# Kernel optimization log

Measured on AMD Instinct MI355X. Metric: run time of the kernel, lower is better.

Reference implementation:

```python
import jax, jax.numpy as jnp
import numpy as np

B, N, D = 4, 8192, 1024
H, DK = 8, 128          # d_k = D // H
FF = 4096
EPS = 1e-5


def setup_inputs() -> dict:
    key = jax.random.key(0)
    ks = jax.random.split(key, 8)
    s = 0.02  # init scale for weights
    return {
        "x": jax.random.normal(ks[0], (B, N, D), jnp.float32),
        "delta_x": jax.random.uniform(ks[1], (N,), jnp.float32),
        # Linear weights stored [in, out] (math-equivalent to torch's x @ W.T)
        "Wq": jax.random.normal(ks[2], (D, D), jnp.float32) * s,
        "bq": jnp.zeros((D,), jnp.float32),
        "Wk": jax.random.normal(ks[3], (D, D), jnp.float32) * s,
        "bk": jnp.zeros((D,), jnp.float32),
        "Wv": jax.random.normal(ks[4], (D, D), jnp.float32) * s,
        "bv": jnp.zeros((D,), jnp.float32),
        # per-head LayerNorm params for K; NOTE: the original code (faithfully
        # reproduced) applies layernorms_K to BOTH key and value in Galerkin mode.
        "gamma_k": jnp.ones((H, DK), jnp.float32),
        "beta_k": jnp.zeros((H, DK), jnp.float32),
        "W1": jax.random.normal(ks[5], (D, FF), jnp.float32) * s,
        "b1": jnp.zeros((FF,), jnp.float32),
        "W2": jax.random.normal(ks[6], (FF, D), jnp.float32) * s,
        "b2": jnp.zeros((D,), jnp.float32),
    }


def _per_head_ln(t, gamma, beta):
    # t: [B, H, N, DK]; torch LayerNorm: biased variance over last dim
    mu = jnp.mean(t, axis=-1, keepdims=True)
    var = jnp.mean(jnp.square(t - mu), axis=-1, keepdims=True)
    t = (t - mu) * jax.lax.rsqrt(var + EPS)
    return t * gamma[None, :, None, :] + beta[None, :, None, :]


def reference(x, delta_x, Wq, bq, Wk, bk, Wv, bv, gamma_k, beta_k, W1, b1, W2, b2):
    b, n, d = x.shape

    def heads(y):  # [b, n, d] -> [b, H, n, DK]
        return y.reshape(b, n, H, DK).transpose(0, 2, 1, 3)

    q = heads(x @ Wq + bq)
    k = heads(x @ Wk + bk)
    v = heads(x @ Wv + bv)

    k = _per_head_ln(k, gamma_k, beta_k)
    v = _per_head_ln(v, gamma_k, beta_k)  # layernorms_K reused on value (as in source)
    k = k * delta_x[None, None, :, None]  # einsum('bhxd,x->bhxd')

    # Galerkin (softmax-free, linear) attention: (K^T V) / N then Q @ (.)
    scores = jnp.einsum("bhnd,bhne->bhde", k, v) / n  # [b,H,DK,DK]
    attn_out = jnp.einsum("bhnd,bhde->bhne", q, scores)  # [b,H,n,DK]
    # (F.dropout in the source treated as identity: inference/eval semantics)

    x = x + attn_out.transpose(0, 2, 1, 3).reshape(b, n, d)  # residual 1
    h = jax.nn.silu(x @ W1 + b1)
    return x + (h @ W2 + b2)  # residual 2
```

## Files before the change

### kernel.cpp

```cpp
#include <hip/hip_runtime.h>
#include <hip/hip_bf16.h>
#include <stdint.h>

#define DEV __device__ __forceinline__

typedef __attribute__((ext_vector_type(8))) short bf16x8;
typedef __attribute__((ext_vector_type(8))) unsigned short u16x8;
typedef __attribute__((ext_vector_type(4))) unsigned short u16x4;
typedef __attribute__((ext_vector_type(4))) float f32x4;

static constexpr int BB = 4, NN = 8192, DD = 1024, HH = 8, DKK = 128, FFF = 4096;
static constexpr int MM = BB * NN;

DEV float bfb2f(unsigned int s) { unsigned int x = s << 16; float f; __builtin_memcpy(&f, &x, 4); return f; }
DEV unsigned short f2bfb(float f) {
    unsigned int x; __builtin_memcpy(&x, &f, 4);
    x += 0x7fffu + ((x >> 16) & 1u);
    return (unsigned short)(x >> 16);
}

DEV void gload_lds16(const void* g, void* l) {
    auto gp = (const __attribute__((address_space(1))) void*)(uintptr_t)g;
    auto lp = (__attribute__((address_space(3))) void*)(unsigned int)(uintptr_t)l;
    __builtin_amdgcn_global_load_lds(gp, lp, 16, 0, 0);
}

__global__ void k_pack_bf16(const float* __restrict__ in, unsigned short* __restrict__ ob, long n) {
    long i = ((long)blockIdx.x * blockDim.x + threadIdx.x) * 8;
    if (i >= n) return;
    f32x4 a = *(const f32x4*)&in[i];
    f32x4 b = *(const f32x4*)&in[i + 4];
    u16x8 o;
    o[0]=f2bfb(a[0]); o[1]=f2bfb(a[1]); o[2]=f2bfb(a[2]); o[3]=f2bfb(a[3]);
    o[4]=f2bfb(b[0]); o[5]=f2bfb(b[1]); o[6]=f2bfb(b[2]); o[7]=f2bfb(b[3]);
    *(u16x8*)&ob[i] = o;
}

DEV void transpose_body(const float* __restrict__ W, unsigned short* __restrict__ WT, int R, int C,
                        int bx, int by, int tid) {
    __shared__ float t[32][33];
    const int r0 = by * 32, c0 = bx * 32;
    const int lr = tid >> 3, lc = (tid & 7) * 4;
    f32x4 v = *(const f32x4*)&W[(long)(r0 + lr) * C + c0 + lc];
    t[lr][lc + 0] = v[0]; t[lr][lc + 1] = v[1]; t[lr][lc + 2] = v[2]; t[lr][lc + 3] = v[3];
    __syncthreads();
    const int oc = tid >> 3, orr = (tid & 7) * 4;
    u16x4 o;
    o[0] = f2bfb(t[orr + 0][oc]); o[1] = f2bfb(t[orr + 1][oc]);
    o[2] = f2bfb(t[orr + 2][oc]); o[3] = f2bfb(t[orr + 3][oc]);
    *(u16x4*)&WT[(long)(c0 + oc) * R + r0 + orr] = o;
}
__global__ void k_transpose(const float* __restrict__ W, unsigned short* __restrict__ WT, int R, int C) {
    transpose_body(W, WT, R, C, blockIdx.x, blockIdx.y, threadIdx.x);
}
__global__ void k_transpose_qkv(const float* __restrict__ Wq, const float* __restrict__ Wk,
                                const float* __restrict__ Wv, unsigned short* __restrict__ WT) {
    const float* W = blockIdx.z == 0 ? Wq : (blockIdx.z == 1 ? Wk : Wv);
    transpose_body(W, WT + (size_t)blockIdx.z * DD * DD, DD, DD, blockIdx.x, blockIdx.y, threadIdx.x);
}

template <int EPI>
__global__ __launch_bounds__(512, 2)
void k_gemm256(const unsigned short* __restrict__ A, int lda,
               const unsigned short* __restrict__ BT, int ldbt,
               const float* __restrict__ bias0, const float* __restrict__ bias1,
               const float* __restrict__ bias2,
               const unsigned short* __restrict__ resb,
               unsigned short* __restrict__ outp0, unsigned short* __restrict__ outp1,
               unsigned short* __restrict__ outp2,
               float* __restrict__ outf,
               int K, int gridx, int npass)
{
    extern __shared__ __align__(128) unsigned short smem[];
    unsigned short* As = smem;
    unsigned short* Bs = smem + 4 * 8192;

    const int wg0 = (blockIdx.x & 7) * 32 + (blockIdx.x >> 3);

    const int tid = threadIdx.x;
    const int lane = tid & 63;
    const int w = tid >> 6;
    const int wm = w >> 2, wn = w & 3;
    const int fr = lane & 15;
    const int kg = lane >> 4;

    const int dl = tid * 16;
    const int soff = dl ^ (((dl >> 7) & 3) << 4);
    const int arow = soff >> 6;
    const int akel = (soff & 63) >> 1;

    int aoff[8], boff[4];
    #pragma unroll
    for (int m = 0; m < 8; ++m) { int o = (wm * 128 + m * 16 + fr) * 64 + kg * 16; aoff[m] = o ^ (((o >> 7) & 3) << 4); }
    #pragma unroll
    for (int n = 0; n < 4; ++n) { int o = (wn * 64 + n * 16 + fr) * 64 + kg * 16; boff[n] = o ^ (((o >> 7) & 3) << 4); }

#define STG_A(base, u, ks, slot) do { \
        const unsigned short* _g = (base) + (long)(u) * 64 + (ks) * 32; \
        gload_lds16(_g,              (slot) + tid * 8); \
        gload_lds16(_g + 128L * lda, (slot) + 4096 + tid * 8); } while (0)
#define STG_B(base, u, ks, slot) do { \
        const unsigned short* _g = (base) + (long)(u) * 64 + (ks) * 32; \
        gload_lds16(_g,               (slot) + tid * 8); \
        gload_lds16(_g + 128L * ldbt, (slot) + 4096 + tid * 8); } while (0)

#define BAR() __builtin_amdgcn_s_barrier()
#define VM8() asm volatile("s_waitcnt vmcnt(8)" ::: "memory")

#define MFMA16(AF, BF, R0) do { \
        __builtin_amdgcn_s_setprio(1); \
        _Pragma("unroll") \
        for (int m = 0; m < 4; ++m) { \
            _Pragma("unroll") \
            for (int n = 0; n < 4; ++n) \
                acc[(R0) + m][n] = __builtin_amdgcn_mfma_f32_16x16x32_bf16(AF[m], BF[n], acc[(R0) + m][n], 0, 0, 0); \
        } \
        __builtin_amdgcn_s_setprio(0); } while (0)

#define DO_TILE(sa0, sa1, sb0, sb1, STG0, STG1, STG2, STG3) do { \
        bf16x8 b0f[4], a0f[4], a1f[4], b1f[4], a2f[4], a3f[4]; \
        _Pragma("unroll") \
        for (int n = 0; n < 4; ++n) b0f[n] = *(const bf16x8*)((const char*)(sb0) + boff[n]); \
        _Pragma("unroll") \
        for (int m = 0; m < 4; ++m) a0f[m] = *(const bf16x8*)((const char*)(sa0) + aoff[m]); \
        _Pragma("unroll") \
        for (int m = 0; m < 4; ++m) a1f[m] = *(const bf16x8*)((const char*)(sa0) + aoff[m + 4]); \
        STG0; \
        BAR(); \
        MFMA16(a0f, b0f, 0); \
        BAR(); \
        STG1; VM8(); \
        BAR(); \
        MFMA16(a1f, b0f, 4); \
        BAR(); \
        _Pragma("unroll") \
        for (int n = 0; n < 4; ++n) b1f[n] = *(const bf16x8*)((const char*)(sb1) + boff[n]); \
        _Pragma("unroll") \
        for (int m = 0; m < 4; ++m) a2f[m] = *(const bf16x8*)((const char*)(sa1) + aoff[m]); \
        _Pragma("unroll") \
        for (int m = 0; m < 4; ++m) a3f[m] = *(const bf16x8*)((const char*)(sa1) + aoff[m + 4]); \
        STG2; \
        BAR(); \
        MFMA16(a2f, b1f, 0); \
        BAR(); \
        STG3; VM8(); \
        BAR(); \
        MFMA16(a3f, b1f, 4); \
        BAR(); \
    } while (0)

    unsigned short* A0 = As;            unsigned short* A1 = As + 8192;
    unsigned short* A2 = As + 16384;    unsigned short* A3 = As + 24576;
    unsigned short* B0 = Bs;            unsigned short* B1 = Bs + 8192;
    unsigned short* B2 = Bs + 16384;    unsigned short* B3 = Bs + 24576;

    const int NT = K >> 6;

    int brow = (wg0 / gridx) * 256;
    int bcol = (wg0 % gridx) * 256;
    const unsigned short* Ab = A + (long)(brow + arow) * lda + akel;
    const unsigned short* Bb = BT + (long)(bcol + arow) * ldbt + akel;
    STG_A(Ab, 0, 0, A0); STG_B(Bb, 0, 0, B0);
    STG_B(Bb, 0, 1, B1); STG_A(Ab, 0, 1, A1);
    STG_A(Ab, 1, 0, A2); STG_B(Bb, 1, 0, B2);
    VM8();
    BAR();

    for (int p = 0; p < npass; ++p) {
        const int wgN = (p + 1 < npass) ? (wg0 + (p + 1) * 256) : wg0;
        const int browN = (wgN / gridx) * 256;
        const int bcolN = (wgN % gridx) * 256;
        const unsigned short* Ab2 = A + (long)(browN + arow) * lda + akel;
        const unsigned short* Bb2 = BT + (long)(bcolN + arow) * ldbt + akel;

        f32x4 acc[8][4] = {};

        for (int t = 0; t + 2 < NT; t += 2) {
            DO_TILE(A0, A1, B0, B1,
                    STG_B(Bb, t + 1, 1, B3), STG_A(Ab, t + 1, 1, A3),
                    STG_A(Ab, t + 2, 0, A0), STG_B(Bb, t + 2, 0, B0));
            DO_TILE(A2, A3, B2, B3,
                    STG_B(Bb, t + 2, 1, B1), STG_A(Ab, t + 2, 1, A1),
                    STG_A(Ab, t + 3, 0, A2), STG_B(Bb, t + 3, 0, B2));
        }
        DO_TILE(A0, A1, B0, B1,
                STG_B(Bb, NT - 1, 1, B3), STG_A(Ab, NT - 1, 1, A3),
                STG_A(Ab2, 0, 0, A0), STG_B(Bb2, 0, 0, B0));
        DO_TILE(A2, A3, B2, B3,
                STG_B(Bb2, 0, 1, B1), STG_A(Ab2, 0, 1, A1),
                STG_A(Ab2, 1, 0, A2), STG_B(Bb2, 1, 0, B2));

        const int q4 = (lane >> 4) * 4;
        if constexpr (EPI == 1) {
            const int mat = bcol >> 10;
            const float* bp = mat == 0 ? bias0 : (mat == 1 ? bias1 : bias2);
            unsigned short* op = mat == 0 ? outp0 : (mat == 1 ? outp1 : outp2);
            const int dc0 = bcol & 1023;
            #pragma unroll
            for (int m = 0; m < 8; ++m)
                #pragma unroll
                for (int n = 0; n < 4; ++n) {
                    const int c = dc0 + wn * 64 + n * 16 + fr;
                    const float bv = bp[c];
                    const int hh = c >> 7, dk = c & 127;
                    #pragma unroll
                    for (int j = 0; j < 4; ++j) {
                        const int r = brow + wm * 128 + m * 16 + q4 + j;
                        const long idx = (((long)(r >> 13) * 8 + hh) * 8192 + (r & 8191)) * 128 + dk;
                        op[idx] = f2bfb(acc[m][n][j] + bv);
                    }
                }
        } else if constexpr (EPI == 2) {
            #pragma unroll
            for (int m = 0; m < 8; ++m)
                #pragma unroll
                for (int n = 0; n < 4; ++n) {
                    const int c = bcol + wn * 64 + n * 16 + fr;
                    const float bv = bias0[c];
                    #pragma unroll
                    for (int j = 0; j < 4; ++j) {
                        const int r = brow + wm * 128 + m * 16 + q4 + j;
                        float v = acc[m][n][j] + bv;
                        v = v / (1.f + __expf(-v));
                        outp0[(long)r * FFF + c] = f2bfb(v);
                    }
                }
        } else {
            #pragma unroll
            for (int m = 0; m < 8; ++m)
                #pragma unroll
                for (int n = 0; n < 4; ++n) {
                    const int c = bcol + wn * 64 + n * 16 + fr;
                    const float bv = bias0[c];
                    #pragma unroll
                    for (int j = 0; j < 4; ++j) {
                        const int r = brow + wm * 128 + m * 16 + q4 + j;
                        float v = acc[m][n][j] + bv + bfb2f(resb[(long)r * DD + c]);
                        outf[(long)r * DD + c] = v;
                    }
                }
        }

        brow = browN; bcol = bcolN; Ab = Ab2; Bb = Bb2;
    }
    asm volatile("s_waitcnt vmcnt(0)" ::: "memory");
#undef DO_TILE
#undef MFMA16
#undef VM8
#undef BAR
#undef STG_A
#undef STG_B
}

template <int EPI>
__global__ __launch_bounds__(256, 2)
void k_gemm(const unsigned short* __restrict__ A, int lda, long sAz,
            const unsigned short* __restrict__ BT, int ldbt, long sBz,
            const unsigned short* __restrict__ resb,
            unsigned short* __restrict__ outp,
            int K)
{
    __shared__ __align__(16) unsigned short As[128 * 32];
    __shared__ __align__(16) unsigned short Bs[128 * 32];
    const int tid = threadIdx.x;
    const int z = blockIdx.z;
    A  += (long)z * sAz;
    BT += (long)z * sBz;
    const int brow = blockIdx.y * 128;
    const int bcol = blockIdx.x * 128;

    const int c0 = tid, c1 = tid + 256;
    const unsigned short* Ap0 = A + (long)(brow + (c0 >> 2)) * lda + (c0 & 3) * 8;
    const unsigned short* Ap1 = A + (long)(brow + (c1 >> 2)) * lda + (c1 & 3) * 8;
    const unsigned short* Bp0 = BT + (long)(bcol + (c0 >> 2)) * ldbt + (c0 & 3) * 8;
    const unsigned short* Bp1 = BT + (long)(bcol + (c1 >> 2)) * ldbt + (c1 & 3) * 8;
    unsigned short* AsD0 = &As[c0 * 8];
    unsigned short* AsD1 = &As[c1 * 8];
    unsigned short* BsD0 = &Bs[c0 * 8];
    unsigned short* BsD1 = &Bs[c1 * 8];

    const int lane = tid & 63;
    const int w = tid >> 6;
    const int wr = (w >> 1) * 64;
    const int wc = (w & 1) * 64;
    const int fr = lane & 15;
    const int fk = (lane >> 4) * 8;

    f32x4 acc[4][4] = {};

    for (int kt = 0; kt < K; kt += 32) {
        gload_lds16(Ap0 + kt, AsD0);
        gload_lds16(Ap1 + kt, AsD1);
        gload_lds16(Bp0 + kt, BsD0);
        gload_lds16(Bp1 + kt, BsD1);
        __syncthreads();
        bf16x8 af[4], bfr[4];
        #pragma unroll
        for (int m = 0; m < 4; ++m) af[m] = *(const bf16x8*)&As[(wr + m * 16 + fr) * 32 + fk];
        #pragma unroll
        for (int n = 0; n < 4; ++n) bfr[n] = *(const bf16x8*)&Bs[(wc + n * 16 + fr) * 32 + fk];
        #pragma unroll
        for (int m = 0; m < 4; ++m)
            #pragma unroll
            for (int n = 0; n < 4; ++n)
                acc[m][n] = __builtin_amdgcn_mfma_f32_16x16x32_bf16(af[m], bfr[n], acc[m][n], 0, 0, 0);
        __syncthreads();
    }

    const int orow = (lane >> 4) * 4;
    #pragma unroll
    for (int m = 0; m < 4; ++m) {
        #pragma unroll
        for (int n = 0; n < 4; ++n) {
            const int d = bcol + wc + n * 16 + fr;
            #pragma unroll
            for (int j = 0; j < 4; ++j) {
                const int r = brow + wr + m * 16 + orow + j;
                if constexpr (EPI == 3) {
                    long xi = ((long)(z >> 3) * NN + r) * DD + (z & 7) * DKK + d;
                    float v = acc[m][n][j] + bfb2f(resb[xi]);
                    outp[xi] = f2bfb(v);
                }
            }
        }
    }
}

__global__ void k_ln(unsigned short* __restrict__ Kb, unsigned short* __restrict__ Vb,
                     const float* __restrict__ gk, const float* __restrict__ bek,
                     const float* __restrict__ dx)
{
    const int tid = threadIdx.x;
    const int lane = tid & 63;
    const long row = (long)blockIdx.x * 4 + (tid >> 6);
    unsigned short* buf = blockIdx.y ? Vb : Kb;
    const int h = (int)((row >> 13) & 7);
    const int n = (int)(row & 8191);
    unsigned int* p = (unsigned int*)(buf + row * 128) + lane;
    const unsigned int u = *p;
    float f0 = bfb2f(u & 0xffffu);
    float f1 = bfb2f(u >> 16);
    float s = f0 + f1, q = f0 * f0 + f1 * f1;
    #pragma unroll
    for (int o = 32; o; o >>= 1) { s += __shfl_xor(s, o); q += __shfl_xor(q, o); }
    const float mean = s * (1.f / 128.f);
    const float var  = q * (1.f / 128.f) - mean * mean;
    const float rstd = rsqrtf(var + 1e-5f);
    const int gi = h * 128 + lane * 2;
    float o0 = (f0 - mean) * rstd * gk[gi]     + bek[gi];
    float o1 = (f1 - mean) * rstd * gk[gi + 1] + bek[gi + 1];
    if (blockIdx.y == 0) { const float dl = dx[n]; o0 *= dl; o1 *= dl; }
    *p = (unsigned int)f2bfb(o0) | ((unsigned int)f2bfb(o1) << 16);
}

__global__ __launch_bounds__(256, 2)
void k_scorespart(const unsigned short* __restrict__ Kb, const unsigned short* __restrict__ Vb,
                  float* __restrict__ part)
{
    __shared__ __align__(16) unsigned short KT[128 * 136];
    __shared__ __align__(16) unsigned short VT[128 * 136];
    const int tid = threadIdx.x;
    const int bh = blockIdx.y, split = blockIdx.x;
    const unsigned short* Kp = Kb + (long)bh * NN * DKK;
    const unsigned short* Vp = Vb + (long)bh * NN * DKK;
    const int lane = tid & 63, w = tid >> 6;
    const int wr = (w >> 1) * 64, wc = (w & 1) * 64, fr = lane & 15, fk = (lane >> 4) * 8;
    const int nrow = tid >> 1, dblk = (tid & 1) * 64;
    f32x4 acc[4][4] = {};
    for (int c = 0; c < 8; ++c) {
        const int n0 = (split * 8 + c) * 128;
        bf16x8 kv[8], vv[8];
        #pragma unroll
        for (int i = 0; i < 8; ++i) {
            kv[i] = *(const bf16x8*)&Kp[(long)(n0 + nrow) * DKK + dblk + i * 8];
            vv[i] = *(const bf16x8*)&Vp[(long)(n0 + nrow) * DKK + dblk + i * 8];
        }
        __syncthreads();
        #pragma unroll
        for (int i = 0; i < 8; ++i)
            #pragma unroll
            for (int j = 0; j < 8; ++j) {
                const int dd = dblk + i * 8 + j;
                KT[dd * 136 + nrow] = (unsigned short)kv[i][j];
                VT[dd * 136 + nrow] = (unsigned short)vv[i][j];
            }
        __syncthreads();
        #pragma unroll
        for (int ks = 0; ks < 4; ++ks) {
            bf16x8 af[4], bfr[4];
            #pragma unroll
            for (int m = 0; m < 4; ++m) af[m] = *(const bf16x8*)&KT[(wr + m * 16 + fr) * 136 + ks * 32 + fk];
            #pragma unroll
            for (int n = 0; n < 4; ++n) bfr[n] = *(const bf16x8*)&VT[(wc + n * 16 + fr) * 136 + ks * 32 + fk];
            #pragma unroll
            for (int m = 0; m < 4; ++m)
                #pragma unroll
                for (int n = 0; n < 4; ++n)
                    acc[m][n] = __builtin_amdgcn_mfma_f32_16x16x32_bf16(af[m], bfr[n], acc[m][n], 0, 0, 0);
        }
    }
    float* P = part + (long)(bh * 8 + split) * 16384;
    const int orow = (lane >> 4) * 4;
    #pragma unroll
    for (int m = 0; m < 4; ++m)
        #pragma unroll
        for (int n = 0; n < 4; ++n)
            #pragma unroll
            for (int j = 0; j < 4; ++j) {
                const int dD = wr + m * 16 + orow + j;
                const int e  = wc + n * 16 + fr;
                P[dD * 128 + e] = acc[m][n][j];
            }
}

__global__ void k_scoresred(const float* __restrict__ part, unsigned short* __restrict__ scT)
{
    const int bh = blockIdx.x, tid = threadIdx.x;
    const float* P = part + (long)bh * 8 * 16384;
    for (int i = tid; i < 16384; i += 256) {
        float s = 0.f;
        #pragma unroll
        for (int sp = 0; sp < 8; ++sp) s += P[sp * 16384 + i];
        const int d = i >> 7, e = i & 127;
        scT[(long)bh * 16384 + e * 128 + d] = f2bfb(s * (1.f / 8192.f));
    }
}

extern "C" void kernel_launch(void* const* d_in, const int* in_sizes, int n_in,
                              void* d_out, int out_size, void* d_ws, size_t ws_size,
                              hipStream_t stream)
{
    const float* x   = (const float*)d_in[0];
    const float* dx  = (const float*)d_in[1];
    const float* Wq  = (const float*)d_in[2];
    const float* bq  = (const float*)d_in[3];
    const float* Wk  = (const float*)d_in[4];
    const float* bk  = (const float*)d_in[5];
    const float* Wv  = (const float*)d_in[6];
    const float* bv  = (const float*)d_in[7];
    const float* gk  = (const float*)d_in[8];
    const float* bek = (const float*)d_in[9];
    const float* W1  = (const float*)d_in[10];
    const float* b1  = (const float*)d_in[11];
    const float* W2  = (const float*)d_in[12];
    const float* b2  = (const float*)d_in[13];
    float* out = (float*)d_out;
    (void)in_sizes; (void)n_in; (void)out_size; (void)ws_size;

    hipFuncSetAttribute((const void*)k_gemm256<1>, hipFuncAttributeMaxDynamicSharedMemorySize, 131072);
    hipFuncSetAttribute((const void*)k_gemm256<2>, hipFuncAttributeMaxDynamicSharedMemorySize, 131072);
    hipFuncSetAttribute((const void*)k_gemm256<3>, hipFuncAttributeMaxDynamicSharedMemorySize, 131072);

    char* ws = (char*)d_ws;
    size_t off = 0;
    auto alloc = [&](size_t bytes) { void* p = ws + off; off += (bytes + 255) & ~(size_t)255; return p; };
    unsigned short* WqkvT = (unsigned short*)alloc((size_t)3 * DD * DD * 2);
    unsigned short* W1T   = (unsigned short*)alloc((size_t)FFF * DD * 2);
    unsigned short* W2T   = (unsigned short*)alloc((size_t)DD * FFF * 2);
    unsigned short* scT   = (unsigned short*)alloc((size_t)32 * 16384 * 2);
    unsigned short* xb    = (unsigned short*)alloc((size_t)MM * DD * 2);
    unsigned short* Kb    = (unsigned short*)alloc((size_t)MM * DD * 2);
    unsigned short* Vb    = (unsigned short*)alloc((size_t)MM * DD * 2);
    unsigned short* x1b   = (unsigned short*)alloc((size_t)MM * DD * 2);
    unsigned short* hb    = xb;
    float* part           = (float*)x1b;
    unsigned short* Qb    = (unsigned short*)out;

    k_pack_bf16<<<dim3(((long)MM * DD) / 8 / 256), 256, 0, stream>>>(x, xb, (long)MM * DD);
    k_transpose_qkv<<<dim3(DD / 32, DD / 32, 3), 256, 0, stream>>>(Wq, Wk, Wv, WqkvT);
    k_transpose<<<dim3(FFF / 32, DD / 32), 256, 0, stream>>>(W1, W1T, DD, FFF);
    k_transpose<<<dim3(DD / 32, FFF / 32), 256, 0, stream>>>(W2, W2T, FFF, DD);

    k_gemm256<1><<<dim3(256), 512, 131072, stream>>>(
        xb, DD, WqkvT, DD, bq, bk, bv, nullptr, Qb, Kb, Vb, nullptr, DD, 3072 / 256, 6);

    k_ln<<<dim3((BB * HH * NN) / 4, 2), 256, 0, stream>>>(Kb, Vb, gk, bek, dx);

    k_scorespart<<<dim3(8, 32), 256, 0, stream>>>(Kb, Vb, part);
    k_scoresred<<<dim3(32), 256, 0, stream>>>(part, scT);

    k_gemm<3><<<dim3(1, NN / 128, BB * HH), 256, 0, stream>>>(Qb, DKK, (long)NN * DKK, scT, DKK, 16384L,
                                                              xb, x1b, DKK);

    for (int c = 0; c < 2; ++c) {
        const unsigned short* xc = x1b + (size_t)c * 16384 * DD;
        k_gemm256<2><<<dim3(256), 512, 131072, stream>>>(
            xc, DD, W1T, DD, b1, nullptr, nullptr, nullptr, hb, nullptr, nullptr, nullptr, DD, FFF / 256, 4);
        k_gemm256<3><<<dim3(256), 512, 131072, stream>>>(
            hb, FFF, W2T, FFF, b2, nullptr, nullptr, xc, nullptr, nullptr, nullptr,
            out + (size_t)c * 16384 * DD, FFF, DD / 256, 1);
    }
}
```

Before: 1.001 ms.

## Restructure persistent GEMM main loop into 4-slot register-prefetched pipeline

Replaces the macro-based half-tile schedule, which had four barriers per 32-wide k-step, with a 4-slot LDS ring. Each region prefetches the next k-slice's fragments into a second register set, issues the global-to-LDS load three slices ahead (crossing into the next tile's pointers at pass boundaries), runs 32 MFMAs, then waits on vmcnt and takes a single barrier. This cuts barrier count and overlaps LDS reads with MFMA. In exchange it holds double the fragment registers, which may strain occupancy at 2 waves per SIMD.

```diff
diff --git a/kernel.cpp b/kernel.cpp
--- a/kernel.cpp
+++ b/kernel.cpp
@@ -89,106 +89,72 @@
     const int arow = soff >> 6;
     const int akel = (soff & 63) >> 1;
 
-    int aoff[8], boff[4];
-    #pragma unroll
-    for (int m = 0; m < 8; ++m) { int o = (wm * 128 + m * 16 + fr) * 64 + kg * 16; aoff[m] = o ^ (((o >> 7) & 3) << 4); }
-    #pragma unroll
-    for (int n = 0; n < 4; ++n) { int o = (wn * 64 + n * 16 + fr) * 64 + kg * 16; boff[n] = o ^ (((o >> 7) & 3) << 4); }
-
-#define STG_A(base, u, ks, slot) do { \
-        const unsigned short* _g = (base) + (long)(u) * 64 + (ks) * 32; \
-        gload_lds16(_g,              (slot) + tid * 8); \
-        gload_lds16(_g + 128L * lda, (slot) + 4096 + tid * 8); } while (0)
-#define STG_B(base, u, ks, slot) do { \
-        const unsigned short* _g = (base) + (long)(u) * 64 + (ks) * 32; \
-        gload_lds16(_g,               (slot) + tid * 8); \
-        gload_lds16(_g + 128L * ldbt, (slot) + 4096 + tid * 8); } while (0)
-
-#define BAR() __builtin_amdgcn_s_barrier()
-#define VM8() asm volatile("s_waitcnt vmcnt(8)" ::: "memory")
-
-#define MFMA16(AF, BF, R0) do { \
-        __builtin_amdgcn_s_setprio(1); \
-        _Pragma("unroll") \
-        for (int m = 0; m < 4; ++m) { \
-            _Pragma("unroll") \
-            for (int n = 0; n < 4; ++n) \
-                acc[(R0) + m][n] = __builtin_amdgcn_mfma_f32_16x16x32_bf16(AF[m], BF[n], acc[(R0) + m][n], 0, 0, 0); \
-        } \
-        __builtin_amdgcn_s_setprio(0); } while (0)
-
-#define DO_TILE(sa0, sa1, sb0, sb1, STG0, STG1, STG2, STG3) do { \
-        bf16x8 b0f[4], a0f[4], a1f[4], b1f[4], a2f[4], a3f[4]; \
-        _Pragma("unroll") \
-        for (int n = 0; n < 4; ++n) b0f[n] = *(const bf16x8*)((const char*)(sb0) + boff[n]); \
-        _Pragma("unroll") \
-        for (int m = 0; m < 4; ++m) a0f[m] = *(const bf16x8*)((const char*)(sa0) + aoff[m]); \
-        _Pragma("unroll") \
-        for (int m = 0; m < 4; ++m) a1f[m] = *(const bf16x8*)((const char*)(sa0) + aoff[m + 4]); \
-        STG0; \
-        BAR(); \
-        MFMA16(a0f, b0f, 0); \
-        BAR(); \
-        STG1; VM8(); \
-        BAR(); \
-        MFMA16(a1f, b0f, 4); \
-        BAR(); \
-        _Pragma("unroll") \
-        for (int n = 0; n < 4; ++n) b1f[n] = *(const bf16x8*)((const char*)(sb1) + boff[n]); \
-        _Pragma("unroll") \
-        for (int m = 0; m < 4; ++m) a2f[m] = *(const bf16x8*)((const char*)(sa1) + aoff[m]); \
-        _Pragma("unroll") \
-        for (int m = 0; m < 4; ++m) a3f[m] = *(const bf16x8*)((const char*)(sa1) + aoff[m + 4]); \
-        STG2; \
-        BAR(); \
-        MFMA16(a2f, b1f, 0); \
-        BAR(); \
-        STG3; VM8(); \
-        BAR(); \
-        MFMA16(a3f, b1f, 4); \
-        BAR(); \
-    } while (0)
-
-    unsigned short* A0 = As;            unsigned short* A1 = As + 8192;
-    unsigned short* A2 = As + 16384;    unsigned short* A3 = As + 24576;
-    unsigned short* B0 = Bs;            unsigned short* B1 = Bs + 8192;
-    unsigned short* B2 = Bs + 16384;    unsigned short* B3 = Bs + 24576;
-
-    const int NT = K >> 6;
+    int ao0 = (wm * 128 + fr) * 64 + kg * 16;  ao0 ^= ((ao0 >> 7) & 3) << 4;
+    int bo0 = (wn * 64  + fr) * 64 + kg * 16;  bo0 ^= ((bo0 >> 7) & 3) << 4;
+    const char* abase = (const char*)As + ao0;
+    const char* bbase = (const char*)Bs + bo0;
+
+    const int NT2 = K >> 5;
 
     int brow = (wg0 / gridx) * 256;
     int bcol = (wg0 % gridx) * 256;
     const unsigned short* Ab = A + (long)(brow + arow) * lda + akel;
     const unsigned short* Bb = BT + (long)(bcol + arow) * ldbt + akel;
-    STG_A(Ab, 0, 0, A0); STG_B(Bb, 0, 0, B0);
-    STG_B(Bb, 0, 1, B1); STG_A(Ab, 0, 1, A1);
-    STG_A(Ab, 1, 0, A2); STG_B(Bb, 1, 0, B2);
-    VM8();
-    BAR();
+
+#define STG(baseA, baseB, ko, slot) do { \
+        gload_lds16((baseA) + (ko),               As + (slot) * 8192 + tid * 8); \
+        gload_lds16((baseA) + (ko) + 128L * lda,  As + (slot) * 8192 + 4096 + tid * 8); \
+        gload_lds16((baseB) + (ko),               Bs + (slot) * 8192 + tid * 8); \
+        gload_lds16((baseB) + (ko) + 128L * ldbt, Bs + (slot) * 8192 + 4096 + tid * 8); } while (0)
+
+    STG(Ab, Bb, 0, 0);
+    STG(Ab, Bb, 32, 1);
+    STG(Ab, Bb, 64, 2);
+    asm volatile("s_waitcnt vmcnt(4)" ::: "memory");
+    __builtin_amdgcn_s_barrier();
+
+    bf16x8 A0f[8], B0f[4], A1f[8], B1f[4];
+    #pragma unroll
+    for (int n = 0; n < 4; ++n) B0f[n] = *(const bf16x8*)(bbase + n * 1024);
+    #pragma unroll
+    for (int m = 0; m < 8; ++m) A0f[m] = *(const bf16x8*)(abase + m * 1024);
+
+#define REGION(CA, CB, NA, NB, SLN, SLG, rr) do { \
+        const bool _inp = (rr) < NT2; \
+        const unsigned short* _sa = _inp ? Ab : Abn; \
+        const unsigned short* _sb = _inp ? Bb : Bbn; \
+        const long _ko = (long)(_inp ? (rr) : (rr) - NT2) * 32; \
+        _Pragma("unroll") \
+        for (int n = 0; n < 4; ++n) NB[n] = *(const bf16x8*)(bbase + (SLN) * 16384 + n * 1024); \
+        _Pragma("unroll") \
+        for (int m = 0; m < 8; ++m) NA[m] = *(const bf16x8*)(abase + (SLN) * 16384 + m * 1024); \
+        STG(_sa, _sb, _ko, SLG); \
+        __builtin_amdgcn_s_setprio(1); \
+        _Pragma("unroll") \
+        for (int m = 0; m < 8; ++m) \
+            _Pragma("unroll") \
+            for (int n = 0; n < 4; ++n) \
+                acc[m][n] = __builtin_amdgcn_mfma_f32_16x16x32_bf16(CA[m], CB[n], acc[m][n], 0, 0, 0); \
+        __builtin_amdgcn_s_setprio(0); \
+        asm volatile("s_waitcnt vmcnt(4)" ::: "memory"); \
+        __builtin_amdgcn_s_barrier(); \
+    } while (0)
 
     for (int p = 0; p < npass; ++p) {
         const int wgN = (p + 1 < npass) ? (wg0 + (p + 1) * 256) : wg0;
         const int browN = (wgN / gridx) * 256;
         const int bcolN = (wgN % gridx) * 256;
-        const unsigned short* Ab2 = A + (long)(browN + arow) * lda + akel;
-        const unsigned short* Bb2 = BT + (long)(bcolN + arow) * ldbt + akel;
+        const unsigned short* Abn = A + (long)(browN + arow) * lda + akel;
+        const unsigned short* Bbn = BT + (long)(bcolN + arow) * ldbt + akel;
 
         f32x4 acc[8][4] = {};
 
-        for (int t = 0; t + 2 < NT; t += 2) {
-            DO_TILE(A0, A1, B0, B1,
-                    STG_B(Bb, t + 1, 1, B3), STG_A(Ab, t + 1, 1, A3),
-                    STG_A(Ab, t + 2, 0, A0), STG_B(Bb, t + 2, 0, B0));
-            DO_TILE(A2, A3, B2, B3,
-                    STG_B(Bb, t + 2, 1, B1), STG_A(Ab, t + 2, 1, A1),
-                    STG_A(Ab, t + 3, 0, A2), STG_B(Bb, t + 3, 0, B2));
+        for (int k = 0; k < NT2; k += 4) {
+            REGION(A0f, B0f, A1f, B1f, 1, 3, k + 3);
+            REGION(A1f, B1f, A0f, B0f, 2, 0, k + 4);
+            REGION(A0f, B0f, A1f, B1f, 3, 1, k + 5);
+            REGION(A1f, B1f, A0f, B0f, 0, 2, k + 6);
         }
-        DO_TILE(A0, A1, B0, B1,
-                STG_B(Bb, NT - 1, 1, B3), STG_A(Ab, NT - 1, 1, A3),
-                STG_A(Ab2, 0, 0, A0), STG_B(Bb2, 0, 0, B0));
-        DO_TILE(A2, A3, B2, B3,
-                STG_B(Bb2, 0, 1, B1), STG_A(Ab2, 0, 1, A1),
-                STG_A(Ab2, 1, 0, A2), STG_B(Bb2, 1, 0, B2));
 
         const int q4 = (lane >> 4) * 4;
         if constexpr (EPI == 1) {
@@ -241,15 +207,11 @@
                 }
         }
 
-        brow = browN; bcol = bcolN; Ab = Ab2; Bb = Bb2;
+        brow = browN; bcol = bcolN; Ab = Abn; Bb = Bbn;
     }
     asm volatile("s_waitcnt vmcnt(0)" ::: "memory");
-#undef DO_TILE
-#undef MFMA16
-#undef VM8
-#undef BAR
-#undef STG_A
-#undef STG_B
+#undef REGION
+#undef STG
 }
 
 template <int EPI>
```

Measured after the change: 1.352 ms. +35.0%, slower.
